# Performance work log

Hardware: AMD Instinct MI355X
Metric: run time of the kernel (lower is better)

The kernel has to match this reference:

```python
import jax, jax.numpy as jnp
import numpy as np

N_LOC = 100000
N_EVT = 100000
N_EDGE = 1600000
F_LOC = 128
F_EVT = 128
QID_DIM = 16
QID_BUCKETS = 4096
HID = 64


def setup_inputs() -> dict:
    key = jax.random.key(0)
    ks = jax.random.split(key, 16)
    s = 0.05
    emb = jax.random.normal(ks[4], (QID_BUCKETS + 1, QID_DIM), jnp.float32) * s
    emb = emb.at[0].set(0.0)  # padding_idx=0
    return {
        "loc_feat": jax.random.normal(ks[0], (N_LOC, F_LOC), jnp.float32),
        "evt_feat": jax.random.normal(ks[1], (N_EVT, F_EVT), jnp.float32),
        "qid_bucket": jax.random.randint(ks[2], (N_LOC,), 0, QID_BUCKETS + 1),
        "edge_index": jax.random.randint(ks[3], (2, N_EDGE), 0, N_LOC),
        "emb": emb,
        "W_loc": jax.random.normal(ks[5], (F_LOC + QID_DIM, HID), jnp.float32) * s,
        "b_loc": jnp.zeros((HID,), jnp.float32),
        "W_evt": jax.random.normal(ks[6], (F_EVT, HID), jnp.float32) * s,
        "b_evt": jnp.zeros((HID,), jnp.float32),
        "W_l": jax.random.normal(ks[7], (HID, HID), jnp.float32) * s,
        "b_l": jnp.zeros((HID,), jnp.float32),
        "W_r": jax.random.normal(ks[8], (HID, HID), jnp.float32) * s,
        "W_h1": jax.random.normal(ks[9], (HID, HID // 2), jnp.float32) * s,
        "b_h1": jnp.zeros((HID // 2,), jnp.float32),
        "W_h2": jax.random.normal(ks[10], (HID // 2, 1), jnp.float32) * s,
        "b_h2": jnp.zeros((1,), jnp.float32),
    }


def reference(loc_feat, evt_feat, qid_bucket, edge_index, emb,
              W_loc, b_loc, W_evt, b_evt, W_l, b_l, W_r,
              W_h1, b_h1, W_h2, b_h2):
    # location input = [x || qid_embedding]
    loc_in = jnp.concatenate([loc_feat, emb[qid_bucket]], axis=1)
    loc_x = jax.nn.relu(loc_in @ W_loc + b_loc)          # [N_loc, H]
    evt_x = jax.nn.relu(evt_feat @ W_evt + b_evt)        # [N_evt, H]

    src, dst = edge_index[0], edge_index[1]
    msg = evt_x[src]                                     # [E, H] gather
    summed = jax.ops.segment_sum(msg, dst, num_segments=N_LOC)
    cnt = jax.ops.segment_sum(jnp.ones((msg.shape[0],), msg.dtype), dst,
                              num_segments=N_LOC)
    mean = summed / jnp.maximum(cnt, 1.0)[:, None]       # scatter-mean aggr

    # SAGEConv: lin_l(mean of neighbors) + lin_r(self)
    loc_x = jax.nn.relu(mean @ W_l + b_l + loc_x @ W_r)

    h = jax.nn.relu(loc_x @ W_h1 + b_h1)
    logits = (h @ W_h2 + b_h2)[:, 0]
    return logits
```

## Files before the change

kernel.cpp:

```cpp
#include <hip/hip_runtime.h>

#define N_LOC 100000
#define N_EVT 100000
#define N_EDGE 1600000
#define NB 391
#define NBIN 391
#define BCAPP 9216
#define TILE 4096
#define RBLK 64
#define DGRID 1563

typedef short bf16x8 __attribute__((ext_vector_type(8)));
typedef float f32x4  __attribute__((ext_vector_type(4)));

__device__ __forceinline__ unsigned bf16_rne(float x) {
    unsigned u = __float_as_uint(x);
    return (u + 0x7fffu + ((u >> 16) & 1u)) >> 16;
}
__device__ __forceinline__ float bf_lo(unsigned u) { return __uint_as_float(u << 16); }
__device__ __forceinline__ float bf_hi(unsigned u) { return __uint_as_float(u & 0xffff0000u); }

__device__ __forceinline__ bf16x8 frag_from_f32(const float* p) {
    float4 v0 = *(const float4*)p;
    float4 v1 = *(const float4*)(p + 4);
    uint4 pk = make_uint4(bf16_rne(v0.x) | (bf16_rne(v0.y) << 16),
                          bf16_rne(v0.z) | (bf16_rne(v0.w) << 16),
                          bf16_rne(v1.x) | (bf16_rne(v1.y) << 16),
                          bf16_rne(v1.z) | (bf16_rne(v1.w) << 16));
    return *(bf16x8*)&pk;
}

__global__ __launch_bounds__(256) void k_prep(
    const float* __restrict__ W_evt, const float* __restrict__ W_loc,
    const float* __restrict__ W_l, const float* __restrict__ W_r,
    const float* __restrict__ W_h1,
    unsigned short* __restrict__ Wt_evt,
    unsigned short* __restrict__ Wt_loc,
    unsigned short* __restrict__ Wt_c,
    unsigned short* __restrict__ Wt_h1,
    unsigned* __restrict__ dummy_row)
{
    const int g0 = blockIdx.x * 256 + threadIdx.x;
    const int gs = gridDim.x * 256;
    for (int idx = g0; idx < 64 * 64; idx += gs) {
        int kp = idx >> 6, c = idx & 63;
        *(unsigned*)&Wt_evt[c * 128 + 2 * kp] =
            bf16_rne(W_evt[(2 * kp + 0) * 64 + c]) |
            (bf16_rne(W_evt[(2 * kp + 1) * 64 + c]) << 16);
    }
    for (int idx = g0; idx < 80 * 64; idx += gs) {
        int kp = idx >> 6, c = idx & 63;
        unsigned v = 0;
        if (kp < 72)
            v = bf16_rne(W_loc[(2 * kp + 0) * 64 + c]) |
                (bf16_rne(W_loc[(2 * kp + 1) * 64 + c]) << 16);
        *(unsigned*)&Wt_loc[c * 160 + 2 * kp] = v;
    }
    for (int idx = g0; idx < 64 * 64; idx += gs) {
        int kp = idx >> 6, c = idx & 63;
        float w0, w1;
        if (kp < 32) { w0 = W_l[(2 * kp + 0) * 64 + c]; w1 = W_l[(2 * kp + 1) * 64 + c]; }
        else { w0 = W_r[(2 * kp - 64 + 0) * 64 + c]; w1 = W_r[(2 * kp - 64 + 1) * 64 + c]; }
        *(unsigned*)&Wt_c[c * 128 + 2 * kp] = bf16_rne(w0) | (bf16_rne(w1) << 16);
    }
    for (int idx = g0; idx < 32 * 32; idx += gs) {
        int kp = idx >> 5, c = idx & 31;
        *(unsigned*)&Wt_h1[c * 64 + 2 * kp] =
            bf16_rne(W_h1[(2 * kp + 0) * 32 + c]) |
            (bf16_rne(W_h1[(2 * kp + 1) * 32 + c]) << 16);
    }
    if (blockIdx.x == 0 && threadIdx.x < 32) dummy_row[threadIdx.x] = 0u;
}

__global__ __launch_bounds__(256) void k_front(
    const float* __restrict__ evt_feat, const unsigned short* __restrict__ Wt_evt,
    const float* __restrict__ b_evt, unsigned short* __restrict__ evtb,
    const float* __restrict__ loc_feat, const int* __restrict__ qid,
    const float* __restrict__ emb, const unsigned short* __restrict__ Wt_loc,
    const float* __restrict__ b_loc, unsigned short* __restrict__ locxb,
    const int* __restrict__ ei, int* __restrict__ cntm, int* __restrict__ offm,
    unsigned* __restrict__ binned)
{
    __shared__ int h[NB];
    __shared__ int sh[512];
    const int bid = blockIdx.x;
    const int t = threadIdx.x;

    if (bid < NBIN) {
        for (int i = t; i < NB; i += 256) h[i] = 0;
        __syncthreads();
        const int e0 = bid * TILE;
        int srcv[16], dstv[16], rnk[16];
#pragma unroll
        for (int j = 0; j < 16; ++j) {
            int e = e0 + j * 256 + t;
            if (e < N_EDGE) {
                srcv[j] = ei[e];
                dstv[j] = ei[N_EDGE + e];
                rnk[j] = atomicAdd(&h[dstv[j] >> 8], 1);
            }
        }
        __syncthreads();
        sh[t] = (t < NB) ? h[t] : 0;
        sh[t + 256] = (t + 256 < NB) ? h[t + 256] : 0;
        __syncthreads();
        for (int off = 1; off < 512; off <<= 1) {
            int v0 = (t >= off) ? sh[t - off] : 0;
            int v1 = (t + 256 >= off) ? sh[t + 256 - off] : 0;
            __syncthreads();
            sh[t] += v0;
            sh[t + 256] += v1;
            __syncthreads();
        }
        for (int i = t; i < NB; i += 256) {
            cntm[(size_t)bid * NB + i] = h[i];
            offm[(size_t)bid * NB + i] = sh[i] - h[i];
        }
#pragma unroll
        for (int j = 0; j < 16; ++j) {
            int e = e0 + j * 256 + t;
            if (e < N_EDGE) {
                int bk = dstv[j] >> 8;
                binned[(size_t)bid * TILE + (sh[bk] - h[bk]) + rnk[j]] =
                    (unsigned)srcv[j] | ((unsigned)(dstv[j] & 255) << 24);
            }
        }
        return;
    }

    const int lane = t & 63;
    const int w = t >> 6;
    const int colL = lane & 15;
    const int kq = lane >> 4;

    int db = bid - NBIN;
    if (db < DGRID) {
        const int gbase = db * RBLK;
        const int arow = min(gbase + 16 * w + colL, N_EVT - 1);
        const float* frow = evt_feat + (size_t)arow * 128;
        f32x4 acc0 = {0.f, 0.f, 0.f, 0.f}, acc1 = acc0, acc2 = acc0, acc3 = acc0;
#pragma unroll
        for (int s = 0; s < 4; ++s) {
            const int kb = s * 32 + kq * 8;
            bf16x8 a  = frag_from_f32(frow + kb);
            bf16x8 b0 = *(const bf16x8*)&Wt_evt[(colL +  0) * 128 + kb];
            bf16x8 b1 = *(const bf16x8*)&Wt_evt[(colL + 16) * 128 + kb];
            bf16x8 b2 = *(const bf16x8*)&Wt_evt[(colL + 32) * 128 + kb];
            bf16x8 b3 = *(const bf16x8*)&Wt_evt[(colL + 48) * 128 + kb];
            acc0 = __builtin_amdgcn_mfma_f32_16x16x32_bf16(a, b0, acc0, 0, 0, 0);
            acc1 = __builtin_amdgcn_mfma_f32_16x16x32_bf16(a, b1, acc1, 0, 0, 0);
            acc2 = __builtin_amdgcn_mfma_f32_16x16x32_bf16(a, b2, acc2, 0, 0, 0);
            acc3 = __builtin_amdgcn_mfma_f32_16x16x32_bf16(a, b3, acc3, 0, 0, 0);
        }
        const float bias0 = b_evt[colL +  0];
        const float bias1 = b_evt[colL + 16];
        const float bias2 = b_evt[colL + 32];
        const float bias3 = b_evt[colL + 48];
        const int rbase = gbase + 16 * w + kq * 4;
#pragma unroll
        for (int j = 0; j < 4; ++j) {
            int grow = rbase + j;
            if (grow < N_EVT) {
                size_t o = (size_t)grow * 64;
                evtb[o + colL +  0] = (unsigned short)bf16_rne(fmaxf(acc0[j] + bias0, 0.f));
                evtb[o + colL + 16] = (unsigned short)bf16_rne(fmaxf(acc1[j] + bias1, 0.f));
                evtb[o + colL + 32] = (unsigned short)bf16_rne(fmaxf(acc2[j] + bias2, 0.f));
                evtb[o + colL + 48] = (unsigned short)bf16_rne(fmaxf(acc3[j] + bias3, 0.f));
            }
        }
        return;
    }

    {
        db -= DGRID;
        const int gbase = db * RBLK;
        const int arow = min(gbase + 16 * w + colL, N_LOC - 1);
        const float* frow = loc_feat + (size_t)arow * 128;
        f32x4 acc0 = {0.f, 0.f, 0.f, 0.f}, acc1 = acc0, acc2 = acc0, acc3 = acc0;
#pragma unroll
        for (int s = 0; s < 4; ++s) {
            const int kb = s * 32 + kq * 8;
            bf16x8 a  = frag_from_f32(frow + kb);
            bf16x8 b0 = *(const bf16x8*)&Wt_loc[(colL +  0) * 160 + kb];
            bf16x8 b1 = *(const bf16x8*)&Wt_loc[(colL + 16) * 160 + kb];
            bf16x8 b2 = *(const bf16x8*)&Wt_loc[(colL + 32) * 160 + kb];
            bf16x8 b3 = *(const bf16x8*)&Wt_loc[(colL + 48) * 160 + kb];
            acc0 = __builtin_amdgcn_mfma_f32_16x16x32_bf16(a, b0, acc0, 0, 0, 0);
            acc1 = __builtin_amdgcn_mfma_f32_16x16x32_bf16(a, b1, acc1, 0, 0, 0);
            acc2 = __builtin_amdgcn_mfma_f32_16x16x32_bf16(a, b2, acc2, 0, 0, 0);
            acc3 = __builtin_amdgcn_mfma_f32_16x16x32_bf16(a, b3, acc3, 0, 0, 0);
        }
        {
            const int kb = 128 + kq * 8;
            bf16x8 a;
            if (kq < 2) {
                int q = qid[arow];
                a = frag_from_f32(emb + (size_t)q * 16 + kq * 8);
            } else {
                uint4 z = make_uint4(0, 0, 0, 0);
                a = *(bf16x8*)&z;
            }
            bf16x8 b0 = *(const bf16x8*)&Wt_loc[(colL +  0) * 160 + kb];
            bf16x8 b1 = *(const bf16x8*)&Wt_loc[(colL + 16) * 160 + kb];
            bf16x8 b2 = *(const bf16x8*)&Wt_loc[(colL + 32) * 160 + kb];
            bf16x8 b3 = *(const bf16x8*)&Wt_loc[(colL + 48) * 160 + kb];
            acc0 = __builtin_amdgcn_mfma_f32_16x16x32_bf16(a, b0, acc0, 0, 0, 0);
            acc1 = __builtin_amdgcn_mfma_f32_16x16x32_bf16(a, b1, acc1, 0, 0, 0);
            acc2 = __builtin_amdgcn_mfma_f32_16x16x32_bf16(a, b2, acc2, 0, 0, 0);
            acc3 = __builtin_amdgcn_mfma_f32_16x16x32_bf16(a, b3, acc3, 0, 0, 0);
        }
        const float bias0 = b_loc[colL +  0];
        const float bias1 = b_loc[colL + 16];
        const float bias2 = b_loc[colL + 32];
        const float bias3 = b_loc[colL + 48];
        const int rbase = gbase + 16 * w + kq * 4;
#pragma unroll
        for (int j = 0; j < 4; ++j) {
            int grow = rbase + j;
            if (grow < N_LOC) {
                size_t o = (size_t)grow * 64;
                locxb[o + colL +  0] = (unsigned short)bf16_rne(fmaxf(acc0[j] + bias0, 0.f));
                locxb[o + colL + 16] = (unsigned short)bf16_rne(fmaxf(acc1[j] + bias1, 0.f));
                locxb[o + colL + 32] = (unsigned short)bf16_rne(fmaxf(acc2[j] + bias2, 0.f));
                locxb[o + colL + 48] = (unsigned short)bf16_rne(fmaxf(acc3[j] + bias3, 0.f));
            }
        }
    }
}

__global__ __launch_bounds__(256) void k_bfill(const int* __restrict__ cntm,
                                               const int* __restrict__ offm,
                                               const unsigned* __restrict__ binned,
                                               int* __restrict__ deg,
                                               int* __restrict__ row_ex,
                                               int* __restrict__ csr) {
    __shared__ int cnt0[NBIN];
    __shared__ int off0[NBIN];
    __shared__ int degl[256];
    __shared__ int sc[256];
    __shared__ int cur[256];
    const int b = blockIdx.x;
    const int t = threadIdx.x;
    for (int i = t; i < NBIN; i += 256) {
        cnt0[i] = cntm[(size_t)i * NB + b];
        off0[i] = offm[(size_t)i * NB + b];
    }
    degl[t] = 0;
    __syncthreads();
    for (int blk = t; blk < NBIN; blk += 256) {
        const int c = cnt0[blk];
        const unsigned* s = binned + (size_t)blk * TILE + off0[blk];
        for (int j = 0; j < c; ++j) atomicAdd(&degl[s[j] >> 24], 1);
    }
    __syncthreads();
    const int v = degl[t];
    const int vpad = (v + 15) & ~15;
    sc[t] = vpad;
    __syncthreads();
    for (int off = 1; off < 256; off <<= 1) {
        int x = (t >= off) ? sc[t - off] : 0;
        __syncthreads();
        sc[t] += x;
        __syncthreads();
    }
    const int ex = b * BCAPP + sc[t] - vpad;
    const int loc = b * 256 + t;
    if (loc < N_LOC) { deg[loc] = v; row_ex[loc] = ex; }
    cur[t] = ex;
    __syncthreads();
    for (int blk = t; blk < NBIN; blk += 256) {
        const int c = cnt0[blk];
        const unsigned* s = binned + (size_t)blk * TILE + off0[blk];
        for (int j = 0; j < c; ++j) {
            unsigned u = s[j];
            int pos = atomicAdd(&cur[u >> 24], 1);
            csr[pos] = (int)(u & 0x00FFFFFFu);
        }
    }
    for (int j = v; j < vpad; ++j) csr[ex + j] = N_EVT;
}

__global__ __launch_bounds__(256) void k_agc(
    const unsigned* __restrict__ evtb, const int* __restrict__ row_ex,
    const int* __restrict__ deg, const int* __restrict__ csr,
    const unsigned* __restrict__ locxb,
    const unsigned short* __restrict__ Wt_c, const float* __restrict__ b_l,
    const unsigned short* __restrict__ Wt_h1, const float* __restrict__ b_h1,
    const float* __restrict__ W_h2, const float* __restrict__ b_h2,
    float* __restrict__ out, int n)
{
    __shared__ unsigned short sA[64 * 136];
    __shared__ unsigned short sX[64 * 72];
    const int t = threadIdx.x;
    const int gbase = blockIdx.x * RBLK;
    const int lane = t & 63;
    const int w = t >> 6;
    for (int idx = t; idx < RBLK * 16; idx += 256) {
        int row = idx >> 4, q4 = idx & 15;
        int grow = gbase + row;
        uint2 p = (grow < n) ? ((const uint2*)locxb)[(size_t)grow * 16 + q4]
                             : make_uint2(0, 0);
        *(uint2*)&sA[row * 136 + 64 + q4 * 4] = p;
    }
    {
        const int half = lane >> 5;
        const int c = lane & 31;
        for (int r = 0; r < 16; ++r) {
            const int loc = gbase + 16 * w + r;
            float a0 = 0.0f, a1 = 0.0f;
            int cnt = 0;
            if (loc < n) {
                const int beg = row_ex[loc];
                cnt = deg[loc];
                const int cntp = (cnt + 15) & ~15;
                for (int i = 0; i < cntp; i += 16) {
                    const int bb = beg + i + half;
                    int s0 = csr[bb +  0];
                    int s1 = csr[bb +  2];
                    int s2 = csr[bb +  4];
                    int s3 = csr[bb +  6];
                    int s4 = csr[bb +  8];
                    int s5 = csr[bb + 10];
                    int s6 = csr[bb + 12];
                    int s7 = csr[bb + 14];
                    unsigned u0 = evtb[(size_t)s0 * 32 + c];
                    unsigned u1 = evtb[(size_t)s1 * 32 + c];
                    unsigned u2 = evtb[(size_t)s2 * 32 + c];
                    unsigned u3 = evtb[(size_t)s3 * 32 + c];
                    unsigned u4 = evtb[(size_t)s4 * 32 + c];
                    unsigned u5 = evtb[(size_t)s5 * 32 + c];
                    unsigned u6 = evtb[(size_t)s6 * 32 + c];
                    unsigned u7 = evtb[(size_t)s7 * 32 + c];
                    a0 += ((bf_lo(u0) + bf_lo(u1)) + (bf_lo(u2) + bf_lo(u3))) +
                          ((bf_lo(u4) + bf_lo(u5)) + (bf_lo(u6) + bf_lo(u7)));
                    a1 += ((bf_hi(u0) + bf_hi(u1)) + (bf_hi(u2) + bf_hi(u3))) +
                          ((bf_hi(u4) + bf_hi(u5)) + (bf_hi(u6) + bf_hi(u7)));
                }
            }
            a0 += __shfl_xor(a0, 32);
            a1 += __shfl_xor(a1, 32);
            const float inv = 1.0f / (float)max(cnt, 1);
            if (lane < 32)
                *(unsigned*)&sA[(16 * w + r) * 136 + 2 * c] =
                    bf16_rne(a0 * inv) | (bf16_rne(a1 * inv) << 16);
        }
    }
    __syncthreads();
    const int colL = lane & 15;
    const int kq = lane >> 4;
    f32x4 acc0 = {0.f, 0.f, 0.f, 0.f}, acc1 = acc0, acc2 = acc0, acc3 = acc0;
#pragma unroll
    for (int s = 0; s < 4; ++s) {
        const int kb = s * 32 + kq * 8;
        bf16x8 a  = *(const bf16x8*)&sA[(16 * w + colL) * 136 + kb];
        bf16x8 b0 = *(const bf16x8*)&Wt_c[(colL +  0) * 128 + kb];
        bf16x8 b1 = *(const bf16x8*)&Wt_c[(colL + 16) * 128 + kb];
        bf16x8 b2 = *(const bf16x8*)&Wt_c[(colL + 32) * 128 + kb];
        bf16x8 b3 = *(const bf16x8*)&Wt_c[(colL + 48) * 128 + kb];
        acc0 = __builtin_amdgcn_mfma_f32_16x16x32_bf16(a, b0, acc0, 0, 0, 0);
        acc1 = __builtin_amdgcn_mfma_f32_16x16x32_bf16(a, b1, acc1, 0, 0, 0);
        acc2 = __builtin_amdgcn_mfma_f32_16x16x32_bf16(a, b2, acc2, 0, 0, 0);
        acc3 = __builtin_amdgcn_mfma_f32_16x16x32_bf16(a, b3, acc3, 0, 0, 0);
    }
    {
        const float bias0 = b_l[colL +  0];
        const float bias1 = b_l[colL + 16];
        const float bias2 = b_l[colL + 32];
        const float bias3 = b_l[colL + 48];
#pragma unroll
        for (int j = 0; j < 4; ++j) {
            int row = 16 * w + kq * 4 + j;
            sX[row * 72 + colL +  0] = (unsigned short)bf16_rne(fmaxf(acc0[j] + bias0, 0.f));
            sX[row * 72 + colL + 16] = (unsigned short)bf16_rne(fmaxf(acc1[j] + bias1, 0.f));
            sX[row * 72 + colL + 32] = (unsigned short)bf16_rne(fmaxf(acc2[j] + bias2, 0.f));
            sX[row * 72 + colL + 48] = (unsigned short)bf16_rne(fmaxf(acc3[j] + bias3, 0.f));
        }
    }
    f32x4 h0 = {0.f, 0.f, 0.f, 0.f}, h1 = h0;
#pragma unroll
    for (int s = 0; s < 2; ++s) {
        const int kb = s * 32 + kq * 8;
        bf16x8 a  = *(const bf16x8*)&sX[(16 * w + colL) * 72 + kb];
        bf16x8 b0 = *(const bf16x8*)&Wt_h1[(colL +  0) * 64 + kb];
        bf16x8 b1 = *(const bf16x8*)&Wt_h1[(colL + 16) * 64 + kb];
        h0 = __builtin_amdgcn_mfma_f32_16x16x32_bf16(a, b0, h0, 0, 0, 0);
        h1 = __builtin_amdgcn_mfma_f32_16x16x32_bf16(a, b1, h1, 0, 0, 0);
    }
    {
        const float bh1c0 = b_h1[colL];
        const float bh1c1 = b_h1[colL + 16];
        const float wh2c0 = W_h2[colL];
        const float wh2c1 = W_h2[colL + 16];
        const float bh2 = b_h2[0];
#pragma unroll
        for (int j = 0; j < 4; ++j) {
            float p = fmaxf(h0[j] + bh1c0, 0.f) * wh2c0 +
                      fmaxf(h1[j] + bh1c1, 0.f) * wh2c1;
            p += __shfl_xor(p, 1);
            p += __shfl_xor(p, 2);
            p += __shfl_xor(p, 4);
            p += __shfl_xor(p, 8);
            int grow = gbase + 16 * w + kq * 4 + j;
            if (colL == 0 && grow < n) out[grow] = p + bh2;
        }
    }
}

extern "C" void kernel_launch(void* const* d_in, const int* in_sizes, int n_in,
                              void* d_out, int out_size, void* d_ws, size_t ws_size,
                              hipStream_t stream) {
    const float* loc_feat = (const float*)d_in[0];
    const float* evt_feat = (const float*)d_in[1];
    const int*   qid      = (const int*)d_in[2];
    const int*   ei       = (const int*)d_in[3];
    const float* emb      = (const float*)d_in[4];
    const float* W_loc    = (const float*)d_in[5];
    const float* b_loc    = (const float*)d_in[6];
    const float* W_evt    = (const float*)d_in[7];
    const float* b_evt    = (const float*)d_in[8];
    const float* W_l      = (const float*)d_in[9];
    const float* b_l      = (const float*)d_in[10];
    const float* W_r      = (const float*)d_in[11];
    const float* W_h1     = (const float*)d_in[12];
    const float* b_h1     = (const float*)d_in[13];
    const float* W_h2     = (const float*)d_in[14];
    const float* b_h2     = (const float*)d_in[15];
    float* out = (float*)d_out;

    char* ws = (char*)d_ws;
    size_t off = 0;
    auto alloc = [&](size_t bytes) -> void* {
        void* p = ws + off;
        off += (bytes + 255) & ~(size_t)255;
        return p;
    };
    unsigned* evtb  = (unsigned*)alloc((size_t)(N_EVT + 1) * 32 * 4);
    unsigned* locxb = (unsigned*)alloc((size_t)N_LOC * 32 * 4);
    unsigned* binned= (unsigned*)alloc((size_t)NBIN * TILE * 4);
    int*   cntm     = (int*)alloc((size_t)NBIN * NB * 4);
    int*   offm     = (int*)alloc((size_t)NBIN * NB * 4);
    int*   deg      = (int*)alloc((size_t)N_LOC * 4);
    int*   row_ex   = (int*)alloc((size_t)(N_LOC + 1) * 4);
    int*   csr      = (int*)alloc((size_t)NB * BCAPP * 4);
    unsigned short* Wt_evt = (unsigned short*)alloc(64 * 128 * 2);
    unsigned short* Wt_loc = (unsigned short*)alloc(64 * 160 * 2);
    unsigned short* Wt_c   = (unsigned short*)alloc(64 * 128 * 2);
    unsigned short* Wt_h1  = (unsigned short*)alloc(32 * 64 * 2);
    (void)ws_size; (void)in_sizes; (void)n_in; (void)out_size;

    k_prep<<<24, 256, 0, stream>>>(W_evt, W_loc, W_l, W_r, W_h1,
                                   Wt_evt, Wt_loc, Wt_c, Wt_h1,
                                   evtb + (size_t)N_EVT * 32);
    k_front<<<NBIN + 2 * DGRID, 256, 0, stream>>>(
        evt_feat, Wt_evt, b_evt, (unsigned short*)evtb,
        loc_feat, qid, emb, Wt_loc, b_loc, (unsigned short*)locxb,
        ei, cntm, offm, binned);
    k_bfill<<<NB, 256, 0, stream>>>(cntm, offm, binned, deg, row_ex, csr);
    k_agc<<<DGRID, 256, 0, stream>>>(evtb, row_ex, deg, csr, locxb,
                                     Wt_c, b_l, Wt_h1, b_h1, W_h2, b_h2,
                                     out, N_LOC);
}
```

Baseline: 151.1 us.

## Double aggregation kernel block to 512 threads and split rows across waves

The fused gather-aggregate-MLP kernel now runs 8 waves per block instead of 4. Each wave aggregates 8 rows instead of 16, and the first MFMA layer splits its output columns across pairs of waves. An extra barrier is added before the head layer, which now runs on only half the waves. The aim is more memory-level parallelism per block in the latency-bound neighbor gather, at the cost of an extra sync and idle waves in the tail.

```diff
diff --git a/kernel.cpp b/kernel.cpp
--- a/kernel.cpp
+++ b/kernel.cpp
@@ -280,7 +280,7 @@
     for (int j = v; j < vpad; ++j) csr[ex + j] = N_EVT;
 }
 
-__global__ __launch_bounds__(256) void k_agc(
+__global__ __launch_bounds__(512) void k_agc(
     const unsigned* __restrict__ evtb, const int* __restrict__ row_ex,
     const int* __restrict__ deg, const int* __restrict__ csr,
     const unsigned* __restrict__ locxb,
@@ -295,7 +295,7 @@
     const int gbase = blockIdx.x * RBLK;
     const int lane = t & 63;
     const int w = t >> 6;
-    for (int idx = t; idx < RBLK * 16; idx += 256) {
+    for (int idx = t; idx < RBLK * 16; idx += 512) {
         int row = idx >> 4, q4 = idx & 15;
         int grow = gbase + row;
         uint2 p = (grow < n) ? ((const uint2*)locxb)[(size_t)grow * 16 + q4]
@@ -305,8 +305,9 @@
     {
         const int half = lane >> 5;
         const int c = lane & 31;
-        for (int r = 0; r < 16; ++r) {
-            const int loc = gbase + 16 * w + r;
+        for (int r = 0; r < 8; ++r) {
+            const int row = 8 * w + r;
+            const int loc = gbase + row;
             float a0 = 0.0f, a1 = 0.0f;
             int cnt = 0;
             if (loc < n) {
@@ -341,52 +342,49 @@
             a1 += __shfl_xor(a1, 32);
             const float inv = 1.0f / (float)max(cnt, 1);
             if (lane < 32)
-                *(unsigned*)&sA[(16 * w + r) * 136 + 2 * c] =
+                *(unsigned*)&sA[row * 136 + 2 * c] =
                     bf16_rne(a0 * inv) | (bf16_rne(a1 * inv) << 16);
         }
     }
     __syncthreads();
+    const int rg = w >> 1;
+    const int ch = w & 1;
     const int colL = lane & 15;
     const int kq = lane >> 4;
-    f32x4 acc0 = {0.f, 0.f, 0.f, 0.f}, acc1 = acc0, acc2 = acc0, acc3 = acc0;
-#pragma unroll
-    for (int s = 0; s < 4; ++s) {
-        const int kb = s * 32 + kq * 8;
-        bf16x8 a  = *(const bf16x8*)&sA[(16 * w + colL) * 136 + kb];
-        bf16x8 b0 = *(const bf16x8*)&Wt_c[(colL +  0) * 128 + kb];
-        bf16x8 b1 = *(const bf16x8*)&Wt_c[(colL + 16) * 128 + kb];
-        bf16x8 b2 = *(const bf16x8*)&Wt_c[(colL + 32) * 128 + kb];
-        bf16x8 b3 = *(const bf16x8*)&Wt_c[(colL + 48) * 128 + kb];
-        acc0 = __builtin_amdgcn_mfma_f32_16x16x32_bf16(a, b0, acc0, 0, 0, 0);
-        acc1 = __builtin_amdgcn_mfma_f32_16x16x32_bf16(a, b1, acc1, 0, 0, 0);
-        acc2 = __builtin_amdgcn_mfma_f32_16x16x32_bf16(a, b2, acc2, 0, 0, 0);
-        acc3 = __builtin_amdgcn_mfma_f32_16x16x32_bf16(a, b3, acc3, 0, 0, 0);
-    }
     {
-        const float bias0 = b_l[colL +  0];
-        const float bias1 = b_l[colL + 16];
-        const float bias2 = b_l[colL + 32];
-        const float bias3 = b_l[colL + 48];
+        f32x4 acc0 = {0.f, 0.f, 0.f, 0.f}, acc1 = acc0;
+#pragma unroll
+        for (int s = 0; s < 4; ++s) {
+            const int kb = s * 32 + kq * 8;
+            bf16x8 a  = *(const bf16x8*)&sA[(16 * rg + colL) * 136 + kb];
+            bf16x8 b0 = *(const bf16x8*)&Wt_c[(ch * 32 + colL +  0) * 128 + kb];
+            bf16x8 b1 = *(const bf16x8*)&Wt_c[(ch * 32 + colL + 16) * 128 + kb];
+            acc0 = __builtin_amdgcn_mfma_f32_16x16x32_bf16(a, b0, acc0, 0, 0, 0);
+            acc1 = __builtin_amdgcn_mfma_f32_16x16x32_bf16(a, b1, acc1, 0, 0, 0);
+        }
+        const float bias0 = b_l[ch * 32 + colL +  0];
+        const float bias1 = b_l[ch * 32 + colL + 16];
 #pragma unroll
         for (int j = 0; j < 4; ++j) {
-            int row = 16 * w + kq * 4 + j;
-            sX[row * 72 + colL +  0] = (unsigned short)bf16_rne(fmaxf(acc0[j] + bias0, 0.f));
-            sX[row * 72 + colL + 16] = (unsigned short)bf16_rne(fmaxf(acc1[j] + bias1, 0.f));
-            sX[row * 72 + colL + 32] = (unsigned short)bf16_rne(fmaxf(acc2[j] + bias2, 0.f));
-            sX[row * 72 + colL + 48] = (unsigned short)bf16_rne(fmaxf(acc3[j] + bias3, 0.f));
-        }
-    }
-    f32x4 h0 = {0.f, 0.f, 0.f, 0.f}, h1 = h0;
-#pragma unroll
-    for (int s = 0; s < 2; ++s) {
-        const int kb = s * 32 + kq * 8;
-        bf16x8 a  = *(const bf16x8*)&sX[(16 * w + colL) * 72 + kb];
-        bf16x8 b0 = *(const bf16x8*)&Wt_h1[(colL +  0) * 64 + kb];
-        bf16x8 b1 = *(const bf16x8*)&Wt_h1[(colL + 16) * 64 + kb];
-        h0 = __builtin_amdgcn_mfma_f32_16x16x32_bf16(a, b0, h0, 0, 0, 0);
-        h1 = __builtin_amdgcn_mfma_f32_16x16x32_bf16(a, b1, h1, 0, 0, 0);
-    }
-    {
+            int row = 16 * rg + kq * 4 + j;
+            sX[row * 72 + ch * 32 + colL +  0] =
+                (unsigned short)bf16_rne(fmaxf(acc0[j] + bias0, 0.f));
+            sX[row * 72 + ch * 32 + colL + 16] =
+                (unsigned short)bf16_rne(fmaxf(acc1[j] + bias1, 0.f));
+        }
+    }
+    __syncthreads();
+    if (ch == 0) {
+        f32x4 h0 = {0.f, 0.f, 0.f, 0.f}, h1 = h0;
+#pragma unroll
+        for (int s = 0; s < 2; ++s) {
+            const int kb = s * 32 + kq * 8;
+            bf16x8 a  = *(const bf16x8*)&sX[(16 * rg + colL) * 72 + kb];
+            bf16x8 b0 = *(const bf16x8*)&Wt_h1[(colL +  0) * 64 + kb];
+            bf16x8 b1 = *(const bf16x8*)&Wt_h1[(colL + 16) * 64 + kb];
+            h0 = __builtin_amdgcn_mfma_f32_16x16x32_bf16(a, b0, h0, 0, 0, 0);
+            h1 = __builtin_amdgcn_mfma_f32_16x16x32_bf16(a, b1, h1, 0, 0, 0);
+        }
         const float bh1c0 = b_h1[colL];
         const float bh1c1 = b_h1[colL + 16];
         const float wh2c0 = W_h2[colL];
@@ -400,7 +398,7 @@
             p += __shfl_xor(p, 2);
             p += __shfl_xor(p, 4);
             p += __shfl_xor(p, 8);
-            int grow = gbase + 16 * w + kq * 4 + j;
+            int grow = gbase + 16 * rg + kq * 4 + j;
             if (colL == 0 && grow < n) out[grow] = p + bh2;
         }
     }
@@ -456,7 +454,7 @@
         loc_feat, qid, emb, Wt_loc, b_loc, (unsigned short*)locxb,
         ei, cntm, offm, binned);
     k_bfill<<<NB, 256, 0, stream>>>(cntm, offm, binned, deg, row_ex, csr);
-    k_agc<<<DGRID, 256, 0, stream>>>(evtb, row_ex, deg, csr, locxb,
+    k_agc<<<DGRID, 512, 0, stream>>>(evtb, row_ex, deg, csr, locxb,
                                      Wt_c, b_l, Wt_h1, b_h1, W_h2, b_h2,
                                      out, N_LOC);
 }
```

Result: faster. 132.9 us (-12.1%).
